# Optimization experiments

Measured on AMD Instinct MI355X. Metric: run time of the kernel, lower is better.

Reference implementation:

```python
import jax, jax.numpy as jnp
import numpy as np

NUM_EXPERTS = 8
TOP_K = 2
N_TOKENS = 4096
HIDDEN = 1024
EXPERT_DIM = 4096


def setup_inputs() -> dict:
    key = jax.random.key(0)
    ks = jax.random.split(key, 4)
    x = jax.random.normal(ks[0], (N_TOKENS, HIDDEN), dtype=jnp.float32)
    Wg = jax.random.normal(ks[1], (HIDDEN, NUM_EXPERTS), dtype=jnp.float32) * 0.02
    bg = jnp.zeros((NUM_EXPERTS,), dtype=jnp.float32)
    W1 = jax.random.normal(ks[2], (NUM_EXPERTS, HIDDEN, EXPERT_DIM), dtype=jnp.float32) * 0.02
    b1 = jnp.zeros((NUM_EXPERTS, EXPERT_DIM), dtype=jnp.float32)
    W2 = jax.random.normal(ks[3], (NUM_EXPERTS, EXPERT_DIM, HIDDEN), dtype=jnp.float32) * 0.02
    b2 = jnp.zeros((NUM_EXPERTS, HIDDEN), dtype=jnp.float32)
    return {"x": x, "Wg": Wg, "bg": bg, "W1": W1, "b1": b1, "W2": W2, "b2": b2}


def reference(x, Wg, bg, W1, b1, W2, b2):
    # Gating: softmax over experts, then top-k routing with renormalized gates.
    gate_probs = jax.nn.softmax(x @ Wg + bg, axis=-1)          # [N, E]
    top_gates, top_idx = jax.lax.top_k(gate_probs, TOP_K)      # [N, K]
    top_gates = top_gates / jnp.sum(top_gates, axis=-1, keepdims=True)
    # Per-(token, expert) combine weight: sum of gates routed to that expert.
    combine = jnp.sum(
        jax.nn.one_hot(top_idx, NUM_EXPERTS, dtype=x.dtype) * top_gates[..., None],
        axis=1,
    )  # [N, E]
    # Expert MLPs: Linear -> ReLU -> Linear (dropout=0 at eval, norm=False).
    out = jnp.zeros_like(x)
    for e in range(NUM_EXPERTS):
        h = jax.nn.relu(x @ W1[e] + b1[e])                      # [N, expert_dim]
        y = h @ W2[e] + b2[e]                                   # [N, hidden]
        out = out + combine[:, e:e + 1] * y
    # Switch-style auxiliary load-balancing loss.
    expert_counts = jnp.sum(gate_probs, axis=0)                 # [E]
    expert_fractions = expert_counts / jnp.sum(expert_counts)
    gate_means = jnp.mean(gate_probs, axis=0)
    aux_loss = NUM_EXPERTS * jnp.sum(expert_fractions * gate_means)
    return out, aux_loss
```

## Files before the change

### kernel.cpp

```cpp
#include <hip/hip_runtime.h>


typedef unsigned short u16;
typedef __bf16 bf16x8 __attribute__((ext_vector_type(8)));
typedef float  f32x4  __attribute__((ext_vector_type(4)));

#define NTOK 4096
#define HID  1024
#define EDIM 4096
#define NEXP 8
#define MAXMT 72

__device__ __forceinline__ u16 f32_bf16(float f) {
  unsigned int u = __float_as_uint(f);
  u += 0x7FFFu + ((u >> 16) & 1u);
  return (u16)(u >> 16);
}

__global__ void gate_kernel(const float* __restrict__ x,
                            const float* __restrict__ Wg,
                            const float* __restrict__ bg,
                            float* __restrict__ combine,
                            float* __restrict__ counts,
                            int* __restrict__ icnt,
                            int* __restrict__ top2idx,
                            float* __restrict__ top2g) {
  __shared__ float lc[NEXP];
  int t = threadIdx.x;
  if (t < NEXP) lc[t] = 0.f;
  __syncthreads();
  int token = blockIdx.x * 4 + (t >> 6);
  int lane = t & 63;
  float s[NEXP] = {};
  const float* xr = x + (size_t)token * HID;
  for (int h = lane; h < HID; h += 64) {
    float xv = xr[h];
    const float* wrow = Wg + (size_t)h * NEXP;
#pragma unroll
    for (int e = 0; e < NEXP; ++e) s[e] += xv * wrow[e];
  }
#pragma unroll
  for (int off = 32; off > 0; off >>= 1) {
#pragma unroll
    for (int e = 0; e < NEXP; ++e) s[e] += __shfl_xor(s[e], off);
  }
  float m = -1e30f;
#pragma unroll
  for (int e = 0; e < NEXP; ++e) { s[e] += bg[e]; m = fmaxf(m, s[e]); }
  float p[NEXP]; float sum = 0.f;
#pragma unroll
  for (int e = 0; e < NEXP; ++e) { p[e] = expf(s[e] - m); sum += p[e]; }
  float inv = 1.f / sum;
#pragma unroll
  for (int e = 0; e < NEXP; ++e) p[e] *= inv;
  int i1 = 0; float g1 = p[0];
#pragma unroll
  for (int e = 1; e < NEXP; ++e) if (p[e] > g1) { g1 = p[e]; i1 = e; }
  int i2 = -1; float g2 = -1.f;
#pragma unroll
  for (int e = 0; e < NEXP; ++e) if (e != i1 && p[e] > g2) { g2 = p[e]; i2 = e; }
  float ginv = 1.f / (g1 + g2);
  if (lane == 0) {
#pragma unroll
    for (int e = 0; e < NEXP; ++e) {
      float c = (e == i1) ? g1 * ginv : (e == i2) ? g2 * ginv : 0.f;
      combine[(size_t)token * NEXP + e] = c;
      atomicAdd(&lc[e], p[e]);
    }
    top2idx[token * 2] = i1; top2idx[token * 2 + 1] = i2;
    top2g[token * 2] = g1 * ginv; top2g[token * 2 + 1] = g2 * ginv;
    atomicAdd(&icnt[i1], 1); atomicAdd(&icnt[i2], 1);
  }
  __syncthreads();
  if (t < NEXP) atomicAdd(&counts[t], lc[t]);
}

__global__ void aux_kernel(const float* __restrict__ counts, float* __restrict__ aux_out) {
  float s = 0.f;
#pragma unroll
  for (int e = 0; e < NEXP; ++e) s += counts[e];
  float a = 0.f;
#pragma unroll
  for (int e = 0; e < NEXP; ++e) a += (counts[e] / s) * (counts[e] / (float)NTOK);
  aux_out[0] = (float)NEXP * a;
}

__global__ void off_kernel(const int* __restrict__ icnt, int* __restrict__ ioff,
                           int* __restrict__ cursor, int* __restrict__ nmtP,
                           int* __restrict__ mtE, int* __restrict__ mtRow0,
                           int* __restrict__ mtValid) {
  int s = 0;
  int loc[NEXP];
  for (int e = 0; e < NEXP; ++e) { loc[e] = s; ioff[e] = s; s += icnt[e]; cursor[e] = 0; }
  int nm = 0;
  for (int e = 0; e < NEXP; ++e) {
    int c = icnt[e];
    int tiles = (c + 127) >> 7;
    for (int mt = 0; mt < tiles; ++mt) {
      mtE[nm] = e; mtRow0[nm] = loc[e] + (mt << 7);
      int v = c - (mt << 7); mtValid[nm] = v > 128 ? 128 : v;
      nm++;
    }
  }
  nmtP[0] = nm;
}

__global__ void fill_kernel(const int* __restrict__ top2idx, const int* __restrict__ ioff,
                            int* __restrict__ cursor, int* __restrict__ tok) {
  int i = blockIdx.x * 256 + threadIdx.x;
  if (i >= NTOK * 2) return;
  int t = i >> 1, k = i & 1;
  int e = top2idx[i];
  int pos = atomicAdd(&cursor[e], 1);
  tok[ioff[e] + pos] = t | (k << 16);
}

__global__ void cvt_kernel(const float* __restrict__ in, u16* __restrict__ out) {
  size_t i = ((size_t)blockIdx.x * 256 + threadIdx.x) * 4;
  float4 v = *(const float4*)(in + i);
  ushort4 o = make_ushort4(f32_bf16(v.x), f32_bf16(v.y), f32_bf16(v.z), f32_bf16(v.w));
  *(ushort4*)(out + i) = o;
}

__global__ void cvtT_kernel(const float* __restrict__ W, u16* __restrict__ WT, int R, int C) {
  __shared__ float tile[32][33];
  int tx = threadIdx.x, ty = threadIdx.y;
  size_t eoff = (size_t)blockIdx.z * R * C;
  const float* Wp = W + eoff;
  u16* WTp = WT + eoff;
  int c0 = blockIdx.x * 32, r0 = blockIdx.y * 32;
#pragma unroll
  for (int i = 0; i < 4; ++i)
    tile[ty + i * 8][tx] = Wp[(size_t)(r0 + ty + i * 8) * C + c0 + tx];
  __syncthreads();
#pragma unroll
  for (int i = 0; i < 4; ++i)
    WTp[(size_t)(c0 + ty + i * 8) * R + r0 + tx] = f32_bf16(tile[tx][ty + i * 8]);
}

template<int MODE>
__global__ __launch_bounds__(256) void gemm_sparse(
    const u16* __restrict__ A, const u16* __restrict__ Wt,
    const int* __restrict__ nmtP, const int* __restrict__ mtE,
    const int* __restrict__ mtRow0, const int* __restrict__ mtValid,
    const int* __restrict__ tok,
    const float* __restrict__ bias, u16* __restrict__ Hout, float* __restrict__ Ypair)
{
  constexpr int KDIM = (MODE == 1) ? HID : EDIM;
  constexpr int NDIM = (MODE == 1) ? EDIM : HID;
  constexpr int NT = NDIM / 128;
  constexpr int NK = KDIM / 32;

  int item = blockIdx.x;
  if (item >= nmtP[0] * NT) return;
  int gmt = item / NT;
  int nt = item - gmt * NT;
  int e = mtE[gmt], row0 = mtRow0[gmt], valid = mtValid[gmt];

  __shared__ __align__(16) u16 As[2][128 * 32];
  __shared__ __align__(16) u16 Bs[2][128 * 32];
  const int t = threadIdx.x;
  const int lane = t & 63;
  const int w = t >> 6;
  const int wr = w >> 1, wc = w & 1;
  const int bn0 = nt << 7;
  const int kq = lane >> 4;
  const int r  = lane & 15;

  const u16* Bb = Wt + ((size_t)e * NDIM + bn0) * KDIM;

  size_t arow[2];
  int srow[2];
#pragma unroll
  for (int c = 0; c < 2; ++c) {
    int idx = c * 256 + t;
    int row = idx >> 2;
    srow[c] = row;
    if (MODE == 1) {
      int rr = (row < valid) ? row : 0;
      arow[c] = (size_t)(tok[row0 + rr] & 0xFFFF) * KDIM;
    } else {
      arow[c] = (size_t)(row0 + row) * KDIM;
    }
  }

  auto stage = [&](int buf, int k0) {
#pragma unroll
    for (int c = 0; c < 2; ++c) {
      int idx = c * 256 + t;
      int kc  = (idx & 3) << 3;
      __builtin_amdgcn_global_load_lds(
          (const __attribute__((address_space(1))) void*)(A + arow[c] + k0 + kc),
          (__attribute__((address_space(3))) void*)(&As[buf][idx * 8]), 16, 0, 0);
      __builtin_amdgcn_global_load_lds(
          (const __attribute__((address_space(1))) void*)(Bb + (size_t)srow[c] * KDIM + k0 + kc),
          (__attribute__((address_space(3))) void*)(&Bs[buf][idx * 8]), 16, 0, 0);
    }
  };

  f32x4 acc[4][4] = {};

  stage(0, 0);
  __syncthreads();
  int cur = 0;
  for (int ks = 0; ks < NK; ++ks) {
    if (ks + 1 < NK) stage(cur ^ 1, (ks + 1) * 32);
    bf16x8 af[4], bfr[4];
#pragma unroll
    for (int f = 0; f < 4; ++f) {
      af[f]  = *(const bf16x8*)(&As[cur][(wr * 64 + f * 16 + r) * 32 + kq * 8]);
      bfr[f] = *(const bf16x8*)(&Bs[cur][(wc * 64 + f * 16 + r) * 32 + kq * 8]);
    }
#pragma unroll
    for (int fm = 0; fm < 4; ++fm) {
#pragma unroll
      for (int fn = 0; fn < 4; ++fn) {
        acc[fn][fm] = __builtin_amdgcn_mfma_f32_16x16x32_bf16(bfr[fn], af[fm], acc[fn][fm], 0, 0, 0);
      }
    }
    __syncthreads();
    cur ^= 1;
  }

  if (MODE == 1) {
#pragma unroll
    for (int fm = 0; fm < 4; ++fm) {
      int lr = wr * 64 + fm * 16 + r;
      if (lr < valid) {
        u16* hrow = Hout + (size_t)(row0 + lr) * EDIM;
#pragma unroll
        for (int fn = 0; fn < 4; ++fn) {
          int col0 = bn0 + wc * 64 + fn * 16 + kq * 4;
          float4 bv = *(const float4*)(bias + (size_t)e * EDIM + col0);
          float v0 = acc[fn][fm][0] + bv.x; v0 = v0 > 0.f ? v0 : 0.f;
          float v1 = acc[fn][fm][1] + bv.y; v1 = v1 > 0.f ? v1 : 0.f;
          float v2 = acc[fn][fm][2] + bv.z; v2 = v2 > 0.f ? v2 : 0.f;
          float v3 = acc[fn][fm][3] + bv.w; v3 = v3 > 0.f ? v3 : 0.f;
          ushort4 h = make_ushort4(f32_bf16(v0), f32_bf16(v1), f32_bf16(v2), f32_bf16(v3));
          *(ushort4*)(hrow + col0) = h;
        }
      }
    }
  } else {
#pragma unroll
    for (int fm = 0; fm < 4; ++fm) {
      int lr = wr * 64 + fm * 16 + r;
      if (lr < valid) {
        int entry = tok[row0 + lr];
        int tt = entry & 0xFFFF, ss = entry >> 16;
        float* yrow = Ypair + ((size_t)ss * NTOK + tt) * HID;
#pragma unroll
        for (int fn = 0; fn < 4; ++fn) {
          int col0 = bn0 + wc * 64 + fn * 16 + kq * 4;
          float4 bv = *(const float4*)(bias + (size_t)e * HID + col0);
          float4 o;
          o.x = acc[fn][fm][0] + bv.x;
          o.y = acc[fn][fm][1] + bv.y;
          o.z = acc[fn][fm][2] + bv.z;
          o.w = acc[fn][fm][3] + bv.w;
          *(float4*)(yrow + col0) = o;
        }
      }
    }
  }
}

__global__ void final_kernel(const float* __restrict__ top2g,
                             const float* __restrict__ Ypair,
                             float* __restrict__ out) {
  size_t idx4 = (size_t)blockIdx.x * 256 + threadIdx.x;
  size_t base = idx4 * 4;
  int t = (int)(base >> 10);
  float g0 = top2g[t * 2], g1 = top2g[t * 2 + 1];
  float4 y0 = *(const float4*)(Ypair + base);
  float4 y1 = *(const float4*)(Ypair + (size_t)NTOK * HID + base);
  float4 o;
  o.x = g0 * y0.x + g1 * y1.x;
  o.y = g0 * y0.y + g1 * y1.y;
  o.z = g0 * y0.z + g1 * y1.z;
  o.w = g0 * y0.w + g1 * y1.w;
  *(float4*)(out + base) = o;
}

__global__ void init_out_kernel(const float* __restrict__ combine,
                                const float* __restrict__ b2,
                                float* __restrict__ out) {
  size_t idx = (size_t)blockIdx.x * 256 + threadIdx.x;
  int i = (int)(idx >> 10), j = (int)(idx & 1023);
  float v = 0.f;
#pragma unroll
  for (int e = 0; e < NEXP; ++e) v += combine[(size_t)i * NEXP + e] * b2[e * HID + j];
  out[idx] = v;
}

template<int MODE>
__global__ __launch_bounds__(256) void gemm_kernel(
    const u16* __restrict__ A, const u16* __restrict__ BT,
    int M, int N, int K,
    const float* __restrict__ bias, u16* __restrict__ Hout,
    const float* __restrict__ combine, int expert, float* __restrict__ Out)
{
  __shared__ __align__(16) u16 As[128 * 32];
  __shared__ __align__(16) u16 Bs[128 * 32];
  const int t = threadIdx.x;
  const int lane = t & 63;
  const int w = t >> 6;
  const int wr = w >> 1, wc = w & 1;
  const int nbn = N >> 7;
  const int bm0 = (int)(blockIdx.x / nbn) << 7;
  const int bn0 = (int)(blockIdx.x % nbn) << 7;
  const int kq = lane >> 4;
  const int r  = lane & 15;
  f32x4 acc[4][4] = {};
  const u16* Ab = A + (size_t)bm0 * K;
  const u16* Bb = BT + (size_t)bn0 * K;
  for (int k0 = 0; k0 < K; k0 += 32) {
    __syncthreads();
#pragma unroll
    for (int c = 0; c < 2; ++c) {
      int idx = c * 256 + t;
      int row = idx >> 2;
      int kc  = (idx & 3) << 3;
      __builtin_amdgcn_global_load_lds(
          (const __attribute__((address_space(1))) void*)(Ab + (size_t)row * K + k0 + kc),
          (__attribute__((address_space(3))) void*)(As + idx * 8), 16, 0, 0);
      __builtin_amdgcn_global_load_lds(
          (const __attribute__((address_space(1))) void*)(Bb + (size_t)row * K + k0 + kc),
          (__attribute__((address_space(3))) void*)(Bs + idx * 8), 16, 0, 0);
    }
    __syncthreads();
    bf16x8 af[4], bfr[4];
#pragma unroll
    for (int f = 0; f < 4; ++f) {
      af[f]  = *(const bf16x8*)(As + (wr * 64 + f * 16 + r) * 32 + kq * 8);
      bfr[f] = *(const bf16x8*)(Bs + (wc * 64 + f * 16 + r) * 32 + kq * 8);
    }
#pragma unroll
    for (int fm = 0; fm < 4; ++fm) {
#pragma unroll
      for (int fn = 0; fn < 4; ++fn) {
        acc[fm][fn] = __builtin_amdgcn_mfma_f32_16x16x32_bf16(af[fm], bfr[fn], acc[fm][fn], 0, 0, 0);
      }
    }
  }
  if (MODE == 1) {
#pragma unroll
    for (int fn = 0; fn < 4; ++fn) {
      int col = bn0 + wc * 64 + fn * 16 + r;
      float bv = bias[col];
#pragma unroll
      for (int fm = 0; fm < 4; ++fm) {
#pragma unroll
        for (int j = 0; j < 4; ++j) {
          int row = bm0 + wr * 64 + fm * 16 + kq * 4 + j;
          float v = acc[fm][fn][j] + bv;
          v = v > 0.f ? v : 0.f;
          Hout[(size_t)row * N + col] = f32_bf16(v);
        }
      }
    }
  } else {
#pragma unroll
    for (int fm = 0; fm < 4; ++fm) {
      float cg[4];
#pragma unroll
      for (int j = 0; j < 4; ++j) {
        int row = bm0 + wr * 64 + fm * 16 + kq * 4 + j;
        cg[j] = combine[(size_t)row * NEXP + expert];
      }
#pragma unroll
      for (int fn = 0; fn < 4; ++fn) {
        int col = bn0 + wc * 64 + fn * 16 + r;
#pragma unroll
        for (int j = 0; j < 4; ++j) {
          int row = bm0 + wr * 64 + fm * 16 + kq * 4 + j;
          Out[(size_t)row * N + col] += cg[j] * acc[fm][fn][j];
        }
      }
    }
  }
}

extern "C" void kernel_launch(void* const* d_in, const int* in_sizes, int n_in,
                              void* d_out, int out_size, void* d_ws, size_t ws_size,
                              hipStream_t stream) {
  (void)in_sizes; (void)n_in; (void)out_size;
  const float* x  = (const float*)d_in[0];
  const float* Wg = (const float*)d_in[1];
  const float* bg = (const float*)d_in[2];
  const float* W1 = (const float*)d_in[3];
  const float* b1 = (const float*)d_in[4];
  const float* W2 = (const float*)d_in[5];
  const float* b2 = (const float*)d_in[6];
  float* out = (float*)d_out;

  char* ws = (char*)d_ws;
  float* counts  = (float*)(ws);
  int*   icnt    = (int*)(ws + 64);
  int*   ioff    = (int*)(ws + 128);
  int*   cursor  = (int*)(ws + 192);
  int*   nmtP    = (int*)(ws + 256);
  int*   mtE     = (int*)(ws + 512);
  int*   mtRow0  = (int*)(ws + 1024);
  int*   mtValid = (int*)(ws + 1536);
  int*   top2idx = (int*)(ws + 4096);
  float* top2g   = (float*)(ws + 36864);
  int*   tok     = (int*)(ws + 69632);
  float* combine = (float*)(ws + 131072);

  const size_t MB = 1024 * 1024;
  u16* xbf = (u16*)(ws + 1 * MB);

  const size_t REQ = 241 * MB;
  bool sparse = ws_size >= REQ;

  hipMemsetAsync(ws, 0, 1024, stream);
  gate_kernel<<<NTOK / 4, 256, 0, stream>>>(x, Wg, bg, combine, counts, icnt, top2idx, top2g);
  aux_kernel<<<1, 1, 0, stream>>>(counts, out + (size_t)NTOK * HID);
  cvt_kernel<<<(NTOK * HID) / 1024, 256, 0, stream>>>(x, xbf);

  if (sparse) {
    u16* w1tA  = (u16*)(ws + 9 * MB);
    u16* w2tA  = (u16*)(ws + 73 * MB);
    u16* H     = (u16*)(ws + 137 * MB);
    float* Ypair = (float*)(ws + 209 * MB);

    cvtT_kernel<<<dim3(EDIM / 32, HID / 32, NEXP), dim3(32, 8), 0, stream>>>(W1, w1tA, HID, EDIM);
    cvtT_kernel<<<dim3(HID / 32, EDIM / 32, NEXP), dim3(32, 8), 0, stream>>>(W2, w2tA, EDIM, HID);
    off_kernel<<<1, 1, 0, stream>>>(icnt, ioff, cursor, nmtP, mtE, mtRow0, mtValid);
    fill_kernel<<<(NTOK * 2 + 255) / 256, 256, 0, stream>>>(top2idx, ioff, cursor, tok);

    gemm_sparse<1><<<MAXMT * (EDIM / 128), 256, 0, stream>>>(
        xbf, w1tA, nmtP, mtE, mtRow0, mtValid, tok, b1, H, nullptr);
    gemm_sparse<2><<<MAXMT * (HID / 128), 256, 0, stream>>>(
        H, w2tA, nmtP, mtE, mtRow0, mtValid, tok, b2, nullptr, Ypair);
    final_kernel<<<(NTOK * HID / 4) / 256, 256, 0, stream>>>(top2g, Ypair, out);
  } else {
    u16* w1t = (u16*)(ws + 9 * MB);
    u16* w2t = (u16*)(ws + 17 * MB);
    u16* H   = (u16*)(ws + 25 * MB);
    init_out_kernel<<<(NTOK * HID) / 256, 256, 0, stream>>>(combine, b2, out);
    for (int e = 0; e < NEXP; ++e) {
      cvtT_kernel<<<dim3(EDIM / 32, HID / 32, 1), dim3(32, 8), 0, stream>>>(
          W1 + (size_t)e * HID * EDIM, w1t, HID, EDIM);
      gemm_kernel<1><<<(NTOK / 128) * (EDIM / 128), 256, 0, stream>>>(
          xbf, w1t, NTOK, EDIM, HID, b1 + (size_t)e * EDIM, H, nullptr, 0, nullptr);
      cvtT_kernel<<<dim3(HID / 32, EDIM / 32, 1), dim3(32, 8), 0, stream>>>(
          W2 + (size_t)e * EDIM * HID, w2t, EDIM, HID);
      gemm_kernel<2><<<(NTOK / 128) * (HID / 128), 256, 0, stream>>>(
          H, w2t, NTOK, HID, EDIM, nullptr, nullptr, combine, e, out);
    }
  }
}
```

Before: 519.4 us.

## Split-K second expert GEMM, remap work items per XCD, widen weight transpose tiles

The down-projection GEMM is split into two K halves. Each half writes its own partial buffer, with Ys1 reusing the now-dead W1 transpose region, and the final kernel sums both halves before applying the gates. This targets the low workgroup count of the N=1024 GEMM. Work items are remapped so consecutive items land on the same XCD, which should improve L2 reuse of weight tiles. The weight transpose/convert kernel now uses 64x64 tiles, float4 loads and a bf16 shared tile, which cuts memory traffic on the conversion pass at the cost of extra partial-buffer writes.

```diff
diff --git a/kernel.cpp b/kernel.cpp
--- a/kernel.cpp
+++ b/kernel.cpp
@@ -122,40 +122,65 @@
   *(ushort4*)(out + i) = o;
 }
 
-__global__ void cvtT_kernel(const float* __restrict__ W, u16* __restrict__ WT, int R, int C) {
-  __shared__ float tile[32][33];
-  int tx = threadIdx.x, ty = threadIdx.y;
+__global__ __launch_bounds__(256) void cvtT_kernel(const float* __restrict__ W,
+                                                   u16* __restrict__ WT, int R, int C) {
+  __shared__ u16 tile[64][66];
+  int t = threadIdx.x;
   size_t eoff = (size_t)blockIdx.z * R * C;
-  const float* Wp = W + eoff;
-  u16* WTp = WT + eoff;
-  int c0 = blockIdx.x * 32, r0 = blockIdx.y * 32;
-#pragma unroll
-  for (int i = 0; i < 4; ++i)
-    tile[ty + i * 8][tx] = Wp[(size_t)(r0 + ty + i * 8) * C + c0 + tx];
+  int c0 = blockIdx.x * 64, r0 = blockIdx.y * 64;
+  const float* Wp = W + eoff + (size_t)r0 * C + c0;
+  u16* WTp = WT + eoff + (size_t)c0 * R + r0;
+#pragma unroll
+  for (int p = 0; p < 4; ++p) {
+    int idx = p * 256 + t;
+    int row = idx >> 4;
+    int col = (idx & 15) * 4;
+    float4 v = *(const float4*)(Wp + (size_t)row * C + col);
+    tile[row][col + 0] = f32_bf16(v.x);
+    tile[row][col + 1] = f32_bf16(v.y);
+    tile[row][col + 2] = f32_bf16(v.z);
+    tile[row][col + 3] = f32_bf16(v.w);
+  }
   __syncthreads();
 #pragma unroll
-  for (int i = 0; i < 4; ++i)
-    WTp[(size_t)(c0 + ty + i * 8) * R + r0 + tx] = f32_bf16(tile[tx][ty + i * 8]);
-}
-
-template<int MODE>
+  for (int p = 0; p < 4; ++p) {
+    int idx = p * 256 + t;
+    int oc = idx >> 4;
+    int orow = (idx & 15) * 4;
+    ushort4 o;
+    o.x = tile[orow + 0][oc];
+    o.y = tile[orow + 1][oc];
+    o.z = tile[orow + 2][oc];
+    o.w = tile[orow + 3][oc];
+    *(ushort4*)(WTp + (size_t)oc * R + orow) = o;
+  }
+}
+
+template<int MODE, int SPLITK>
 __global__ __launch_bounds__(256) void gemm_sparse(
     const u16* __restrict__ A, const u16* __restrict__ Wt,
     const int* __restrict__ nmtP, const int* __restrict__ mtE,
     const int* __restrict__ mtRow0, const int* __restrict__ mtValid,
     const int* __restrict__ tok,
-    const float* __restrict__ bias, u16* __restrict__ Hout, float* __restrict__ Ypair)
+    const float* __restrict__ bias, u16* __restrict__ Hout,
+    float* __restrict__ Y0, float* __restrict__ Y1)
 {
   constexpr int KDIM = (MODE == 1) ? HID : EDIM;
   constexpr int NDIM = (MODE == 1) ? EDIM : HID;
   constexpr int NT = NDIM / 128;
-  constexpr int NK = KDIM / 32;
-
-  int item = blockIdx.x;
-  if (item >= nmtP[0] * NT) return;
-  int gmt = item / NT;
-  int nt = item - gmt * NT;
-  int e = mtE[gmt], row0 = mtRow0[gmt], valid = mtValid[gmt];
+  constexpr int NK = KDIM / 32 / SPLITK;
+
+  const int nwg = gridDim.x;
+  const int q = nwg >> 3, rr8 = nwg & 7;
+  const int xcd = blockIdx.x & 7, jj = blockIdx.x >> 3;
+  int item = (xcd < rr8 ? xcd * (q + 1) : rr8 * (q + 1) + (xcd - rr8) * q) + jj;
+
+  if (item >= nmtP[0] * NT * SPLITK) return;
+  const int gmt = item / (NT * SPLITK);
+  const int sk  = (item / NT) % SPLITK;
+  const int nt  = item % NT;
+  const int e = mtE[gmt], row0 = mtRow0[gmt], valid = mtValid[gmt];
+  const int kbeg = sk * (KDIM / SPLITK);
 
   __shared__ __align__(16) u16 As[2][128 * 32];
   __shared__ __align__(16) u16 Bs[2][128 * 32];
@@ -177,8 +202,8 @@
     int row = idx >> 2;
     srow[c] = row;
     if (MODE == 1) {
-      int rr = (row < valid) ? row : 0;
-      arow[c] = (size_t)(tok[row0 + rr] & 0xFFFF) * KDIM;
+      int rw = (row < valid) ? row : 0;
+      arow[c] = (size_t)(tok[row0 + rw] & 0xFFFF) * KDIM;
     } else {
       arow[c] = (size_t)(row0 + row) * KDIM;
     }
@@ -200,11 +225,11 @@
 
   f32x4 acc[4][4] = {};
 
-  stage(0, 0);
+  stage(0, kbeg);
   __syncthreads();
   int cur = 0;
   for (int ks = 0; ks < NK; ++ks) {
-    if (ks + 1 < NK) stage(cur ^ 1, (ks + 1) * 32);
+    if (ks + 1 < NK) stage(cur ^ 1, kbeg + (ks + 1) * 32);
     bf16x8 af[4], bfr[4];
 #pragma unroll
     for (int f = 0; f < 4; ++f) {
@@ -242,22 +267,30 @@
       }
     }
   } else {
+    float* Yb = (sk == 0) ? Y0 : Y1;
 #pragma unroll
     for (int fm = 0; fm < 4; ++fm) {
       int lr = wr * 64 + fm * 16 + r;
       if (lr < valid) {
         int entry = tok[row0 + lr];
         int tt = entry & 0xFFFF, ss = entry >> 16;
-        float* yrow = Ypair + ((size_t)ss * NTOK + tt) * HID;
+        float* yrow = Yb + ((size_t)ss * NTOK + tt) * HID;
 #pragma unroll
         for (int fn = 0; fn < 4; ++fn) {
           int col0 = bn0 + wc * 64 + fn * 16 + kq * 4;
-          float4 bv = *(const float4*)(bias + (size_t)e * HID + col0);
           float4 o;
-          o.x = acc[fn][fm][0] + bv.x;
-          o.y = acc[fn][fm][1] + bv.y;
-          o.z = acc[fn][fm][2] + bv.z;
-          o.w = acc[fn][fm][3] + bv.w;
+          if (sk == 0) {
+            float4 bv = *(const float4*)(bias + (size_t)e * HID + col0);
+            o.x = acc[fn][fm][0] + bv.x;
+            o.y = acc[fn][fm][1] + bv.y;
+            o.z = acc[fn][fm][2] + bv.z;
+            o.w = acc[fn][fm][3] + bv.w;
+          } else {
+            o.x = acc[fn][fm][0];
+            o.y = acc[fn][fm][1];
+            o.z = acc[fn][fm][2];
+            o.w = acc[fn][fm][3];
+          }
           *(float4*)(yrow + col0) = o;
         }
       }
@@ -266,19 +299,22 @@
 }
 
 __global__ void final_kernel(const float* __restrict__ top2g,
-                             const float* __restrict__ Ypair,
+                             const float* __restrict__ Ys0,
+                             const float* __restrict__ Ys1,
                              float* __restrict__ out) {
   size_t idx4 = (size_t)blockIdx.x * 256 + threadIdx.x;
   size_t base = idx4 * 4;
   int t = (int)(base >> 10);
   float g0 = top2g[t * 2], g1 = top2g[t * 2 + 1];
-  float4 y0 = *(const float4*)(Ypair + base);
-  float4 y1 = *(const float4*)(Ypair + (size_t)NTOK * HID + base);
+  float4 a0 = *(const float4*)(Ys0 + base);
+  float4 b0 = *(const float4*)(Ys1 + base);
+  float4 a1 = *(const float4*)(Ys0 + (size_t)NTOK * HID + base);
+  float4 b1 = *(const float4*)(Ys1 + (size_t)NTOK * HID + base);
   float4 o;
-  o.x = g0 * y0.x + g1 * y1.x;
-  o.y = g0 * y0.y + g1 * y1.y;
-  o.z = g0 * y0.z + g1 * y1.z;
-  o.w = g0 * y0.w + g1 * y1.w;
+  o.x = g0 * (a0.x + b0.x) + g1 * (a1.x + b1.x);
+  o.y = g0 * (a0.y + b0.y) + g1 * (a1.y + b1.y);
+  o.z = g0 * (a0.z + b0.z) + g1 * (a1.z + b1.z);
+  o.w = g0 * (a0.w + b0.w) + g1 * (a1.w + b1.w);
   *(float4*)(out + base) = o;
 }
 
@@ -420,32 +456,33 @@
   cvt_kernel<<<(NTOK * HID) / 1024, 256, 0, stream>>>(x, xbf);
 
   if (sparse) {
-    u16* w1tA  = (u16*)(ws + 9 * MB);
-    u16* w2tA  = (u16*)(ws + 73 * MB);
-    u16* H     = (u16*)(ws + 137 * MB);
-    float* Ypair = (float*)(ws + 209 * MB);
-
-    cvtT_kernel<<<dim3(EDIM / 32, HID / 32, NEXP), dim3(32, 8), 0, stream>>>(W1, w1tA, HID, EDIM);
-    cvtT_kernel<<<dim3(HID / 32, EDIM / 32, NEXP), dim3(32, 8), 0, stream>>>(W2, w2tA, EDIM, HID);
+    u16* w1tA    = (u16*)(ws + 9 * MB);
+    u16* w2tA    = (u16*)(ws + 73 * MB);
+    u16* H       = (u16*)(ws + 137 * MB);
+    float* Ys0   = (float*)(ws + 209 * MB);
+    float* Ys1   = (float*)(ws + 9 * MB);
+
+    cvtT_kernel<<<dim3(EDIM / 64, HID / 64, NEXP), 256, 0, stream>>>(W1, w1tA, HID, EDIM);
+    cvtT_kernel<<<dim3(HID / 64, EDIM / 64, NEXP), 256, 0, stream>>>(W2, w2tA, EDIM, HID);
     off_kernel<<<1, 1, 0, stream>>>(icnt, ioff, cursor, nmtP, mtE, mtRow0, mtValid);
     fill_kernel<<<(NTOK * 2 + 255) / 256, 256, 0, stream>>>(top2idx, ioff, cursor, tok);
 
-    gemm_sparse<1><<<MAXMT * (EDIM / 128), 256, 0, stream>>>(
-        xbf, w1tA, nmtP, mtE, mtRow0, mtValid, tok, b1, H, nullptr);
-    gemm_sparse<2><<<MAXMT * (HID / 128), 256, 0, stream>>>(
-        H, w2tA, nmtP, mtE, mtRow0, mtValid, tok, b2, nullptr, Ypair);
-    final_kernel<<<(NTOK * HID / 4) / 256, 256, 0, stream>>>(top2g, Ypair, out);
+    gemm_sparse<1, 1><<<MAXMT * (EDIM / 128), 256, 0, stream>>>(
+        xbf, w1tA, nmtP, mtE, mtRow0, mtValid, tok, b1, H, nullptr, nullptr);
+    gemm_sparse<2, 2><<<MAXMT * (HID / 128) * 2, 256, 0, stream>>>(
+        H, w2tA, nmtP, mtE, mtRow0, mtValid, tok, b2, nullptr, Ys0, Ys1);
+    final_kernel<<<(NTOK * HID / 4) / 256, 256, 0, stream>>>(top2g, Ys0, Ys1, out);
   } else {
     u16* w1t = (u16*)(ws + 9 * MB);
     u16* w2t = (u16*)(ws + 17 * MB);
     u16* H   = (u16*)(ws + 25 * MB);
     init_out_kernel<<<(NTOK * HID) / 256, 256, 0, stream>>>(combine, b2, out);
     for (int e = 0; e < NEXP; ++e) {
-      cvtT_kernel<<<dim3(EDIM / 32, HID / 32, 1), dim3(32, 8), 0, stream>>>(
+      cvtT_kernel<<<dim3(EDIM / 64, HID / 64, 1), 256, 0, stream>>>(
           W1 + (size_t)e * HID * EDIM, w1t, HID, EDIM);
       gemm_kernel<1><<<(NTOK / 128) * (EDIM / 128), 256, 0, stream>>>(
           xbf, w1t, NTOK, EDIM, HID, b1 + (size_t)e * EDIM, H, nullptr, 0, nullptr);
-      cvtT_kernel<<<dim3(HID / 32, EDIM / 32, 1), dim3(32, 8), 0, stream>>>(
+      cvtT_kernel<<<dim3(HID / 64, EDIM / 64, 1), 256, 0, stream>>>(
           W2 + (size_t)e * EDIM * HID, w2t, EDIM, HID);
       gemm_kernel<2><<<(NTOK / 128) * (HID / 128), 256, 0, stream>>>(
           H, w2t, NTOK, HID, EDIM, nullptr, nullptr, combine, e, out);
```

Result: faster. 499.9 us (-3.8%).
